# Kernel optimization log

Measured on AMD Instinct MI355X. Metric: run time of the kernel, lower is better.

The kernel has to match this reference:

```python
import jax, jax.numpy as jnp
import numpy as np

EPS = 1e-5
EMBED_DIM = 1024
CTX_DIM = 768
NUM_HEADS = 16
DH = EMBED_DIM // NUM_HEADS
# Faithful to torch source: embed_dim // num_heads ** 0.5 parses as embed_dim // (num_heads**0.5)
SCALE = EMBED_DIM // (NUM_HEADS ** 0.5)  # = 256.0


def ws_conv1x1(x, w, b, mask):
    # weight-standardized 1x1 conv1d: w [O, I, 1], x [B, I, T]
    w2 = w[..., 0]
    mu = jnp.mean(w2, axis=1, keepdims=True)
    var = jnp.var(w2, axis=1, keepdims=True)
    wn = (w2 - mu) * jax.lax.rsqrt(var + EPS)
    y = jnp.einsum('oi,bit->bot', wn, x) + b[None, :, None]
    if mask is not None:
        y = jnp.where(mask, y, 0.0)  # mask [B,1,T] bool
    return y


def layernorm(x, g, b):
    # normalize over last axis
    mu = jnp.mean(x, axis=-1, keepdims=True)
    var = jnp.var(x, axis=-1, keepdims=True)
    return (x - mu) * jax.lax.rsqrt(var + EPS) * g + b


def setup_inputs() -> dict:
    key = jax.random.key(0)
    ks = jax.random.split(key, 16)
    B, T, S = 4, 1024, 1024
    inp = {
        'x': jax.random.normal(ks[0], (B, EMBED_DIM, T), dtype=jnp.float32),
        'context': jax.random.normal(ks[1], (B, CTX_DIM, S), dtype=jnp.float32),
        'mask': jax.random.randint(ks[2], (B, 1, T), 0, 2).astype(bool),
        'mask_ctx': jax.random.randint(ks[3], (B, 1, S), 0, 2).astype(bool),
        'qw': jax.random.normal(ks[4], (EMBED_DIM, EMBED_DIM, 1), dtype=jnp.float32) * 0.02,
        'qb': jnp.zeros((EMBED_DIM,), jnp.float32),
        'kw': jax.random.normal(ks[5], (EMBED_DIM, CTX_DIM, 1), dtype=jnp.float32) * 0.02,
        'kb': jnp.zeros((EMBED_DIM,), jnp.float32),
        'vw': jax.random.normal(ks[6], (EMBED_DIM, CTX_DIM, 1), dtype=jnp.float32) * 0.02,
        'vb': jnp.zeros((EMBED_DIM,), jnp.float32),
        'ow': jax.random.normal(ks[7], (EMBED_DIM, EMBED_DIM, 1), dtype=jnp.float32) * 0.02,
        'ob': jnp.zeros((EMBED_DIM,), jnp.float32),
        'gq': jnp.ones((DH,), jnp.float32), 'bq': jnp.zeros((DH,), jnp.float32),
        'gk': jnp.ones((DH,), jnp.float32), 'bk': jnp.zeros((DH,), jnp.float32),
        'gv': jnp.ones((DH,), jnp.float32), 'bv': jnp.zeros((DH,), jnp.float32),
    }
    return inp


def reference(x, context, mask, mask_ctx, qw, qb, kw, kb, vw, vb, ow, ob, gq, bq, gk, bk, gv, bv):
    B, E, T = x.shape
    S = context.shape[-1]
    q = ws_conv1x1(x, qw, qb, mask)            # [B,E,T]
    k = ws_conv1x1(context, kw, kb, mask_ctx)  # [B,E,S]
    v = ws_conv1x1(context, vw, vb, mask_ctx)  # [B,E,S]
    # split heads -> [B,H,dh,L]
    q = q.reshape(B, NUM_HEADS, DH, T)
    k = k.reshape(B, NUM_HEADS, DH, S)
    v = v.reshape(B, NUM_HEADS, DH, S)
    # middle_norm: LayerNorm over dh (applied on transposed layout)
    q = jnp.swapaxes(layernorm(jnp.swapaxes(q, -1, -2), gq, bq), -1, -2)
    k = jnp.swapaxes(layernorm(jnp.swapaxes(k, -1, -2), gk, bk), -1, -2)
    v = jnp.swapaxes(layernorm(jnp.swapaxes(v, -1, -2), gv, bv), -1, -2)
    # scores: k^T @ q -> [B,H,S,T]
    scores = jnp.einsum('bhds,bhdt->bhst', k, q) / SCALE
    scores = jnp.where(mask[:, :, None, :], scores, -1e9)  # mask over query dim T
    scores = jax.nn.softmax(scores, axis=-1)               # softmax over T (as in source)
    scores = jnp.where(mask_ctx[:, :, :, None], scores, 0.0)
    out = jnp.einsum('bhds,bhst->bhdt', v, scores)          # v @ scores -> [B,H,dh,T]
    out = out.reshape(B, E, T)
    out = ws_conv1x1(out, ow, ob, mask) + x
    return out
```

## Files before the change

### kernel.cpp

```cpp
#include <hip/hip_runtime.h>

#define NB 4
#define TT 1024
#define SS 1024
#define EE 1024
#define CCH 768
#define NH 16
#define DHH 64
#define EPSF 1e-5f
#define QSCALE (1.4426950408889634f / 256.0f)

typedef unsigned short u16;
typedef __attribute__((ext_vector_type(8))) short short8;
typedef __attribute__((ext_vector_type(8))) unsigned short u16x8;
typedef __attribute__((ext_vector_type(4))) unsigned short u16x4;
typedef __attribute__((ext_vector_type(4))) float f32x4;

__device__ __forceinline__ u16 f2bu(float f) {
    union { float f; unsigned u; } x; x.f = f;
    unsigned r = x.u + 0x7fffu + ((x.u >> 16) & 1u);
    return (u16)(r >> 16);
}
__device__ __forceinline__ float bu2f(u16 u) {
    union { unsigned u; float f; } x; x.u = ((unsigned)u) << 16; return x.f;
}

#if __has_builtin(__builtin_amdgcn_exp2f)
#define EXP2(x) __builtin_amdgcn_exp2f(x)
#else
#define EXP2(x) exp2f(x)
#endif

#define MFMA16(a, b, c) __builtin_amdgcn_mfma_f32_16x16x32_bf16((a), (b), (c), 0, 0, 0)

#define PREP_WS_END   4096
#define PREP_SCAN_END (PREP_WS_END + 8)
#define PREP_TR_END   (PREP_SCAN_END + 1792)
#define PREP_FILL_END (PREP_TR_END + 4096)

__global__ __launch_bounds__(256) void prep(
    const float* __restrict__ qw, const float* __restrict__ kw,
    const float* __restrict__ vw, const float* __restrict__ ow,
    u16* __restrict__ wqn, u16* __restrict__ wkn,
    u16* __restrict__ wvn, u16* __restrict__ won,
    const float* __restrict__ x, const float* __restrict__ ctx,
    const int* __restrict__ mask, const int* __restrict__ mask_ctx,
    u16* __restrict__ xc, u16* __restrict__ cc,
    int* __restrict__ tIdx, int* __restrict__ sIdx,
    int* __restrict__ cntQ, int* __restrict__ cntK,
    float* __restrict__ outF) {
    __shared__ float tile[64][65];
    __shared__ int spos[64], smask[64], wtoti[4];
    __shared__ float sa[4], sb2[4], smean, srstd;
    int bid = blockIdx.x, tid = threadIdx.x;

    if (bid < PREP_WS_END) {
        int mat = bid >> 10, row = bid & 1023;
        const float* w = mat == 0 ? qw : (mat == 1 ? kw : (mat == 2 ? vw : ow));
        u16* wn = mat == 0 ? wqn : (mat == 1 ? wkn : (mat == 2 ? wvn : won));
        int I = (mat == 1 || mat == 2) ? CCH : EE;
        const float* wr = w + (size_t)row * I;
        float s = 0.f, s2 = 0.f;
        for (int i = tid; i < I; i += 256) { float v = wr[i]; s += v; s2 += v * v; }
#pragma unroll
        for (int off = 32; off > 0; off >>= 1) { s += __shfl_down(s, off); s2 += __shfl_down(s2, off); }
        int wid = tid >> 6;
        if ((tid & 63) == 0) { sa[wid] = s; sb2[wid] = s2; }
        __syncthreads();
        if (tid == 0) {
            float ts = sa[0] + sa[1] + sa[2] + sa[3];
            float ts2 = sb2[0] + sb2[1] + sb2[2] + sb2[3];
            float mean = ts / (float)I;
            float var = ts2 / (float)I - mean * mean;
            smean = mean; srstd = rsqrtf(var + EPSF);
        }
        __syncthreads();
        float mean = smean, r = srstd;
        u16* wo = wn + (size_t)row * I;
        for (int i = tid; i < I; i += 256) wo[i] = f2bu((wr[i] - mean) * r);
        return;
    }
    if (bid < PREP_SCAN_END) {
        int t = bid - PREP_WS_END;
        int which = t & 1, b = t >> 1;
        const int* m = (which ? mask_ctx : mask) + b * 1024;
        int* idx = (which ? sIdx : tIdx) + b * 1024;
        int* cnt = (which ? cntK : cntQ) + b;
        int base = tid * 4;
        int v[4]; int s = 0;
#pragma unroll
        for (int i = 0; i < 4; i++) { v[i] = m[base + i] ? 1 : 0; s += v[i]; }
        int lane = tid & 63, wid = tid >> 6;
        int inc = s;
#pragma unroll
        for (int off = 1; off < 64; off <<= 1) {
            int o = __shfl_up(inc, off);
            if (lane >= off) inc += o;
        }
        if (lane == 63) wtoti[wid] = inc;
        __syncthreads();
        int woff = 0;
        for (int i = 0; i < wid; i++) woff += wtoti[i];
        int p = woff + inc - s;
#pragma unroll
        for (int i = 0; i < 4; i++) {
            if (v[i]) idx[p] = base + i;
            p += v[i];
        }
        if (tid == 255) *cnt = p;
        return;
    }
    if (bid < PREP_TR_END) {
        int t = bid - PREP_SCAN_END;
        int xb = t & 15; int rem = t >> 4;
        int yy = rem % 28, b = rem / 28;
        int mat = yy < 16 ? 0 : 1;
        int r0 = (mat == 0 ? yy : yy - 16) * 64;
        int R = mat == 0 ? EE : CCH;
        const float* in = mat == 0 ? x : ctx;
        const int* m = (mat == 0 ? mask : mask_ctx) + (size_t)b * 1024;
        u16* out = mat == 0 ? xc : cc;
        int c0 = xb * 64;
        const float* ip = in + (size_t)b * R * 1024;
        u16* op = out + (size_t)b * R * 1024;
#pragma unroll
        for (int mm = 0; mm < 16; mm++) {
            int id = tid + 256 * mm; int r = id >> 6, c = id & 63;
            tile[r][c] = ip[(size_t)(r0 + r) * 1024 + c0 + c];
        }
        int base = tid * 4;
        int v[4]; int s = 0;
#pragma unroll
        for (int i = 0; i < 4; i++) { v[i] = m[base + i] ? 1 : 0; s += v[i]; }
        int lane = tid & 63, wid = tid >> 6;
        int inc = s;
#pragma unroll
        for (int off = 1; off < 64; off <<= 1) {
            int o = __shfl_up(inc, off);
            if (lane >= off) inc += o;
        }
        if (lane == 63) wtoti[wid] = inc;
        __syncthreads();
        int woff = 0;
        for (int i = 0; i < wid; i++) woff += wtoti[i];
        int p = woff + inc - s;
#pragma unroll
        for (int i = 0; i < 4; i++) {
            int g = base + i;
            if (g >= c0 && g < c0 + 64) { spos[g - c0] = p; smask[g - c0] = v[i]; }
            p += v[i];
        }
        __syncthreads();
#pragma unroll
        for (int mm = 0; mm < 16; mm++) {
            int id = tid + 256 * mm; int rr = id >> 6, cc2 = id & 63;
            if (smask[rr])
                op[(size_t)spos[rr] * R + r0 + cc2] = f2bu(tile[cc2][rr]);
        }
        return;
    }
    {
        int f = bid - PREP_TR_END;
        int b = f >> 10, o = f & 1023;
        const float* xr = x + ((size_t)b * EE + o) * TT;
        float* orow = outF + ((size_t)b * EE + o) * TT;
        const int* mrow = mask + (size_t)b * TT;
        int4 mv = ((const int4*)mrow)[tid];
        float4 xv = ((const float4*)xr)[tid];
        int t4 = tid * 4;
        if (!mv.x) orow[t4 + 0] = xv.x;
        if (!mv.y) orow[t4 + 1] = xv.y;
        if (!mv.z) orow[t4 + 2] = xv.z;
        if (!mv.w) orow[t4 + 3] = xv.w;
    }
}

__device__ __forceinline__ void gemm_core(
    const u16* __restrict__ A, const u16* __restrict__ Bp, int I,
    int o0, int l0, u16 (*at)[72], u16 (*bt)[72], f32x4 (&acc)[4][2]) {
    int tid = threadIdx.x;
    int w = tid >> 6, lane = tid & 63, quad = lane >> 4, l16 = lane & 15;
    int wm = w & 1, wn = w >> 1;
    int rA = tid >> 3, cA = (tid & 7) * 8;
    u16x8 ra[2][4], rb[2][2];
#pragma unroll
    for (int p = 0; p < 2; p++) {
        int kb = p * 64;
#pragma unroll
        for (int m = 0; m < 4; m++)
            ra[p][m] = *(const u16x8*)&A[(size_t)(o0 + rA + 32 * m) * I + kb + cA];
#pragma unroll
        for (int m = 0; m < 2; m++)
            rb[p][m] = *(const u16x8*)&Bp[(size_t)(l0 + rA + 32 * m) * I + kb + cA];
    }
    for (int k0 = 0; k0 < I; k0 += 128) {
#pragma unroll
        for (int half = 0; half < 2; half++) {
            __syncthreads();
#pragma unroll
            for (int m = 0; m < 4; m++) *(u16x8*)&at[rA + 32 * m][cA] = ra[half][m];
#pragma unroll
            for (int m = 0; m < 2; m++) *(u16x8*)&bt[rA + 32 * m][cA] = rb[half][m];
            __syncthreads();
            int kpre = k0 + half * 64 + 128;
            if (kpre < I) {
#pragma unroll
                for (int m = 0; m < 4; m++)
                    ra[half][m] = *(const u16x8*)&A[(size_t)(o0 + rA + 32 * m) * I + kpre + cA];
#pragma unroll
                for (int m = 0; m < 2; m++)
                    rb[half][m] = *(const u16x8*)&Bp[(size_t)(l0 + rA + 32 * m) * I + kpre + cA];
            }
#pragma unroll
            for (int ks = 0; ks < 64; ks += 32) {
                short8 af[4], bf[2];
#pragma unroll
                for (int i = 0; i < 4; i++)
                    af[i] = *(const short8*)&at[wm * 64 + i * 16 + l16][ks + quad * 8];
#pragma unroll
                for (int j = 0; j < 2; j++)
                    bf[j] = *(const short8*)&bt[wn * 32 + j * 16 + l16][ks + quad * 8];
#pragma unroll
                for (int mt = 0; mt < 4; mt++)
#pragma unroll
                    for (int nt = 0; nt < 2; nt++)
                        acc[mt][nt] = MFMA16(af[mt], bf[nt], acc[mt][nt]);
            }
        }
    }
}

__device__ __forceinline__ void gemm_core64(
    const u16* __restrict__ A, const u16* __restrict__ Bp, int I,
    int o0, int l0, u16 (*at)[72], u16 (*bt)[72], f32x4 (&acc)[4]) {
    int tid = threadIdx.x;
    int w = tid >> 6, lane = tid & 63, quad = lane >> 4, l16 = lane & 15;
    int rA = tid >> 3, cA = (tid & 7) * 8;
    u16x8 ra[2][2], rb[2][2];
#pragma unroll
    for (int p = 0; p < 2; p++) {
        int kb = p * 64;
#pragma unroll
        for (int m = 0; m < 2; m++) {
            ra[p][m] = *(const u16x8*)&A[(size_t)(o0 + rA + 32 * m) * I + kb + cA];
            rb[p][m] = *(const u16x8*)&Bp[(size_t)(l0 + rA + 32 * m) * I + kb + cA];
        }
    }
    for (int k0 = 0; k0 < I; k0 += 128) {
#pragma unroll
        for (int half = 0; half < 2; half++) {
            __syncthreads();
#pragma unroll
            for (int m = 0; m < 2; m++) {
                *(u16x8*)&at[rA + 32 * m][cA] = ra[half][m];
                *(u16x8*)&bt[rA + 32 * m][cA] = rb[half][m];
            }
            __syncthreads();
            int kpre = k0 + half * 64 + 128;
            if (kpre < I) {
#pragma unroll
                for (int m = 0; m < 2; m++) {
                    ra[half][m] = *(const u16x8*)&A[(size_t)(o0 + rA + 32 * m) * I + kpre + cA];
                    rb[half][m] = *(const u16x8*)&Bp[(size_t)(l0 + rA + 32 * m) * I + kpre + cA];
                }
            }
#pragma unroll
            for (int ks = 0; ks < 64; ks += 32) {
                short8 bf = *(const short8*)&bt[w * 16 + l16][ks + quad * 8];
#pragma unroll
                for (int mt = 0; mt < 4; mt++) {
                    short8 af = *(const short8*)&at[mt * 16 + l16][ks + quad * 8];
                    acc[mt] = MFMA16(af, bf, acc[mt]);
                }
            }
        }
    }
}

__global__ __launch_bounds__(256) void proj_qkv(
    const u16* __restrict__ wq, const u16* __restrict__ wk, const u16* __restrict__ wv,
    const u16* __restrict__ xc, const u16* __restrict__ cc,
    const float* __restrict__ qb, const float* __restrict__ kb, const float* __restrict__ vbi,
    const int* __restrict__ cntQ, const int* __restrict__ cntK,
    const float* __restrict__ gq, const float* __restrict__ bq,
    const float* __restrict__ gk, const float* __restrict__ bk,
    u16* __restrict__ qc, u16* __restrict__ kc, u16* __restrict__ yv) {
    int mat = blockIdx.x >> 3;
    int o0 = (blockIdx.x & 7) * 128;
    int l0 = blockIdx.y * 64;
    int b = blockIdx.z;
    int limit = (mat == 0) ? cntQ[b] : cntK[b];
    if (l0 >= limit) return;
    __shared__ u16 at[128][72];
    __shared__ u16 bt[64][72];
    __shared__ float sg[64], sbe[64], sbias[128];
    int tid = threadIdx.x;
    int w = tid >> 6, lane = tid & 63, quad = lane >> 4, l16 = lane & 15;
    int wm = w & 1, wn = w >> 1;
    const u16* A = mat == 0 ? wq : (mat == 1 ? wk : wv);
    const u16* BT = mat == 0 ? xc : cc;
    const float* bias = mat == 0 ? qb : (mat == 1 ? kb : vbi);
    int I = mat == 0 ? EE : CCH;
    if (mat < 2 && tid < 64) {
        sg[tid] = (mat == 0 ? gq : gk)[tid];
        sbe[tid] = (mat == 0 ? bq : bk)[tid];
    }
    if (tid < 128) sbias[tid] = bias[o0 + tid];

    f32x4 acc[4][2] = {};
    gemm_core(A, BT + (size_t)b * 1024 * I, I, o0, l0, at, bt, acc);

    if (mat < 2) {
        u16* outT = mat == 0 ? qc : kc;
        float scale = mat == 0 ? QSCALE : 1.0f;
        int h = (o0 >> 6) + wm;
        int bh = b * NH + h;
#pragma unroll
        for (int nt = 0; nt < 2; nt++) {
            int l = l0 + wn * 32 + nt * 16 + l16;
            float vbuf[16];
            float s = 0.f;
#pragma unroll
            for (int mt = 0; mt < 4; mt++)
#pragma unroll
                for (int reg = 0; reg < 4; reg++) {
                    float v = acc[mt][nt][reg] + sbias[wm * 64 + mt * 16 + quad * 4 + reg];
                    vbuf[mt * 4 + reg] = v; s += v;
                }
            s += __shfl_xor(s, 16); s += __shfl_xor(s, 32);
            float mean = s * (1.f / 64);
            float s2 = 0.f;
#pragma unroll
            for (int i = 0; i < 16; i++) { float dv = vbuf[i] - mean; s2 += dv * dv; }
            s2 += __shfl_xor(s2, 16); s2 += __shfl_xor(s2, 32);
            float r = rsqrtf(s2 * (1.f / 64) + EPSF);
            if (l < limit) {
                u16* op = outT + ((size_t)bh * 1024 + l) * 64;
#pragma unroll
                for (int mt = 0; mt < 4; mt++) {
                    u16x4 pk;
#pragma unroll
                    for (int reg = 0; reg < 4; reg++) {
                        int d = mt * 16 + quad * 4 + reg;
                        pk[reg] = f2bu(((vbuf[mt * 4 + reg] - mean) * r * sg[d] + sbe[d]) * scale);
                    }
                    *(u16x4*)&op[mt * 16 + quad * 4] = pk;
                }
            }
        }
    } else {
#pragma unroll
        for (int nt = 0; nt < 2; nt++) {
            int l = l0 + wn * 32 + nt * 16 + l16;
            if (l < limit) {
#pragma unroll
                for (int mt = 0; mt < 4; mt++)
#pragma unroll
                    for (int reg = 0; reg < 4; reg++) {
                        int o = o0 + wm * 64 + mt * 16 + quad * 4 + reg;
                        float v = acc[mt][nt][reg] + sbias[wm * 64 + mt * 16 + quad * 4 + reg];
                        yv[((size_t)b * EE + o) * 1024 + l] = f2bu(v);
                    }
            }
        }
    }
}

__global__ __launch_bounds__(256) void attn_stats_mfma(
    const u16* __restrict__ qc, const u16* __restrict__ kc,
    const int* __restrict__ cntQ, const int* __restrict__ cntK,
    const float* __restrict__ gv, const float* __restrict__ bv,
    const u16* __restrict__ yv, u16* __restrict__ vc) {
    int s0 = blockIdx.x * 64, h = blockIdx.y, b = blockIdx.z;
    int Sc = cntK[b], Tc = cntQ[b];
    if (s0 >= Sc) return;
    __shared__ u16 kt[64][72];
    __shared__ u16 qt[64][72];
    __shared__ float lp[4][64];
    int tid = threadIdx.x;
    int w = tid >> 6, lane = tid & 63, quad = lane >> 4, l16 = lane & 15;
    int head = b * NH + h;
    const u16* kp = kc + (size_t)head * SS * DHH;
    const u16* qp = qc + (size_t)head * TT * DHH;
    int rA = tid >> 3, cA = (tid & 7) * 8;
#pragma unroll
    for (int m = 0; m < 2; m++)
        *(u16x8*)&kt[rA + 32 * m][cA] = *(const u16x8*)&kp[(size_t)(s0 + rA + 32 * m) * DHH + cA];
    u16x8 rq[2][2];
#pragma unroll
    for (int p = 0; p < 2; p++)
#pragma unroll
        for (int m = 0; m < 2; m++)
            rq[p][m] = *(const u16x8*)&qp[(size_t)(p * 64 + rA + 32 * m) * DHH + cA];
    float rl[4][4] = {};
    for (int t0 = 0; t0 < Tc; t0 += 128) {
#pragma unroll
        for (int half = 0; half < 2; half++) {
            int tb = t0 + half * 64;
            __syncthreads();
#pragma unroll
            for (int m = 0; m < 2; m++) *(u16x8*)&qt[rA + 32 * m][cA] = rq[half][m];
            __syncthreads();
            int tpre = tb + 128;
            if (tpre < TT) {
#pragma unroll
                for (int m = 0; m < 2; m++)
                    rq[half][m] = *(const u16x8*)&qp[(size_t)(tpre + rA + 32 * m) * DHH + cA];
            }
            int tcol = tb + w * 16 + l16;
            f32x4 acc[4] = {};
#pragma unroll
            for (int ks = 0; ks < 64; ks += 32) {
                short8 bf = *(const short8*)&qt[w * 16 + l16][ks + quad * 8];
#pragma unroll
                for (int mt = 0; mt < 4; mt++) {
                    short8 af = *(const short8*)&kt[mt * 16 + l16][ks + quad * 8];
                    acc[mt] = MFMA16(af, bf, acc[mt]);
                }
            }
            if (tcol < Tc) {
#pragma unroll
                for (int mt = 0; mt < 4; mt++)
#pragma unroll
                    for (int reg = 0; reg < 4; reg++)
                        rl[mt][reg] += EXP2(acc[mt][reg]);
            }
        }
    }
#pragma unroll
    for (int mt = 0; mt < 4; mt++) {
#pragma unroll
        for (int reg = 0; reg < 4; reg++) {
            float v = rl[mt][reg];
            v += __shfl_xor(v, 1); v += __shfl_xor(v, 2);
            v += __shfl_xor(v, 4); v += __shfl_xor(v, 8);
            if (l16 == 0) lp[w][mt * 16 + quad * 4 + reg] = v;
        }
    }
    __syncthreads();
    if (tid < 64 && s0 + tid < Sc) {
        int spos = s0 + tid;
        float lv = lp[0][tid] + lp[1][tid] + lp[2][tid] + lp[3][tid];
        float wsc = lv > 0.f ? (1.f / lv) : 0.f;
        const u16* vin = yv + ((size_t)b * EE + h * 64) * SS + spos;
        u16* vout = vc + ((size_t)b * EE + h * 64) * SS + spos;
        float sm = 0.f, s2 = 0.f;
        float vals[DHH];
#pragma unroll
        for (int d = 0; d < DHH; d++) {
            float v = bu2f(vin[(size_t)d * SS]);
            vals[d] = v; sm += v; s2 += v * v;
        }
        float mean = sm * (1.f / DHH);
        float var = s2 * (1.f / DHH) - mean * mean;
        float r = rsqrtf(var + EPSF);
#pragma unroll
        for (int d = 0; d < DHH; d++)
            vout[(size_t)d * SS] = f2bu(((vals[d] - mean) * r * gv[d] + bv[d]) * wsc);
    }
}

__global__ __launch_bounds__(256) void attn_pv_mfma(
    const u16* __restrict__ qc, const u16* __restrict__ kc, const u16* __restrict__ vc,
    const int* __restrict__ cntQ, const int* __restrict__ cntK,
    u16* __restrict__ ac) {
    int t0 = blockIdx.x * 64, h = blockIdx.y, b = blockIdx.z;
    int Tc = cntQ[b], Sc = cntK[b];
    if (t0 >= Tc) return;
    __shared__ u16 qt[64][72];
    __shared__ u16 kt[64][72];
    __shared__ u16 vt[64][72];
    __shared__ u16 pt[64][72];
    int tid = threadIdx.x;
    int w = tid >> 6, lane = tid & 63, quad = lane >> 4, l16 = lane & 15;
    int head = b * NH + h;
    const u16* qp = qc + (size_t)head * TT * DHH;
    const u16* kp = kc + (size_t)head * SS * DHH;
    const u16* vp = vc + ((size_t)head * DHH) * SS;
    int rA = tid >> 3, cA = (tid & 7) * 8;
#pragma unroll
    for (int m = 0; m < 2; m++)
        *(u16x8*)&qt[rA + 32 * m][cA] = *(const u16x8*)&qp[(size_t)(t0 + rA + 32 * m) * DHH + cA];
    u16x8 rk[2][2], rv[2][2];
#pragma unroll
    for (int p = 0; p < 2; p++)
#pragma unroll
        for (int m = 0; m < 2; m++) {
            rk[p][m] = *(const u16x8*)&kp[(size_t)(p * 64 + rA + 32 * m) * DHH + cA];
            rv[p][m] = *(const u16x8*)&vp[(size_t)(rA + 32 * m) * SS + p * 64 + cA];
        }
    int tl = w * 16 + l16;

    f32x4 oacc[4] = {};
    for (int s0 = 0; s0 < Sc; s0 += 128) {
#pragma unroll
        for (int half = 0; half < 2; half++) {
            int sb = s0 + half * 64;
            if (sb >= Sc) break;
            __syncthreads();
#pragma unroll
            for (int m = 0; m < 2; m++) {
                *(u16x8*)&kt[rA + 32 * m][cA] = rk[half][m];
                *(u16x8*)&vt[rA + 32 * m][cA] = rv[half][m];
            }
            __syncthreads();
            int spre = sb + 128;
            if (spre < SS) {
#pragma unroll
                for (int m = 0; m < 2; m++) {
                    rk[half][m] = *(const u16x8*)&kp[(size_t)(spre + rA + 32 * m) * DHH + cA];
                    rv[half][m] = *(const u16x8*)&vp[(size_t)(rA + 32 * m) * SS + spre + cA];
                }
            }
            f32x4 acc[4] = {};
#pragma unroll
            for (int ks = 0; ks < 64; ks += 32) {
                short8 bf = *(const short8*)&qt[tl][ks + quad * 8];
#pragma unroll
                for (int mt = 0; mt < 4; mt++) {
                    short8 af = *(const short8*)&kt[mt * 16 + l16][ks + quad * 8];
                    acc[mt] = MFMA16(af, bf, acc[mt]);
                }
            }
#pragma unroll
            for (int mt = 0; mt < 4; mt++) {
                u16x4 pk;
#pragma unroll
                for (int reg = 0; reg < 4; reg++) {
                    int sl = mt * 16 + quad * 4 + reg;
                    pk[reg] = (sb + sl < Sc) ? f2bu(EXP2(acc[mt][reg])) : (u16)0;
                }
                *(u16x4*)&pt[tl][mt * 16 + quad * 4] = pk;
            }
#pragma unroll
            for (int ks = 0; ks < 64; ks += 32) {
                short8 bf = *(const short8*)&pt[tl][ks + quad * 8];
#pragma unroll
                for (int mt = 0; mt < 4; mt++) {
                    short8 af = *(const short8*)&vt[mt * 16 + l16][ks + quad * 8];
                    oacc[mt] = MFMA16(af, bf, oacc[mt]);
                }
            }
        }
    }
    __syncthreads();
#pragma unroll
    for (int mt = 0; mt < 4; mt++) {
        u16x4 pk;
#pragma unroll
        for (int reg = 0; reg < 4; reg++) pk[reg] = f2bu(oacc[mt][reg]);
        *(u16x4*)&pt[tl][mt * 16 + quad * 4] = pk;
    }
    __syncthreads();
#pragma unroll
    for (int i = 0; i < 2; i++) {
        int id = tid * 2 + i;
        int r = id >> 3, c = (id & 7) * 8;
        if (t0 + r < Tc)
            *(u16x8*)&ac[((size_t)b * TT + t0 + r) * EE + h * 64 + c] =
                *(const u16x8*)&pt[r][c];
    }
}

__global__ __launch_bounds__(256) void proj_o(
    const u16* __restrict__ won, const u16* __restrict__ ac,
    const float* __restrict__ obi, const int* __restrict__ tIdx,
    const int* __restrict__ cntQ, const float* __restrict__ x,
    float* __restrict__ out) {
    int o0 = blockIdx.x * 64, l0 = blockIdx.y * 64, b = blockIdx.z;
    int Tc = cntQ[b];
    if (l0 >= Tc) return;
    __shared__ u16 at[64][72];
    __shared__ u16 bt[64][72];
    __shared__ float sbias[64];
    __shared__ int stre[64];
    int tid = threadIdx.x;
    int w = tid >> 6, lane = tid & 63, quad = lane >> 4, l16 = lane & 15;
    if (tid < 64) {
        sbias[tid] = obi[o0 + tid];
        stre[tid] = tIdx[(size_t)b * 1024 + l0 + tid];
    }
    f32x4 acc[4] = {};
    gemm_core64(won, ac + (size_t)b * TT * EE, EE, o0, l0, at, bt, acc);
    int l = l0 + w * 16 + l16;
    if (l < Tc) {
        int treal = stre[w * 16 + l16];
#pragma unroll
        for (int mt = 0; mt < 4; mt++)
#pragma unroll
            for (int reg = 0; reg < 4; reg++) {
                int o = o0 + mt * 16 + quad * 4 + reg;
                size_t off = ((size_t)b * EE + o) * TT + treal;
                out[off] = acc[mt][reg] + sbias[mt * 16 + quad * 4 + reg] + x[off];
            }
    }
}

extern "C" void kernel_launch(void* const* d_in, const int* in_sizes, int n_in,
                              void* d_out, int out_size, void* d_ws, size_t ws_size,
                              hipStream_t stream) {
    const float* x        = (const float*)d_in[0];
    const float* ctx      = (const float*)d_in[1];
    const int*   mask     = (const int*)d_in[2];
    const int*   mask_ctx = (const int*)d_in[3];
    const float* qw  = (const float*)d_in[4];
    const float* qbi = (const float*)d_in[5];
    const float* kw  = (const float*)d_in[6];
    const float* kbi = (const float*)d_in[7];
    const float* vw  = (const float*)d_in[8];
    const float* vbi = (const float*)d_in[9];
    const float* ow  = (const float*)d_in[10];
    const float* obi = (const float*)d_in[11];
    const float* gq = (const float*)d_in[12];
    const float* bq = (const float*)d_in[13];
    const float* gk = (const float*)d_in[14];
    const float* bk = (const float*)d_in[15];
    const float* gv = (const float*)d_in[16];
    const float* bv = (const float*)d_in[17];

    u16* p = (u16*)d_ws;
    u16* wqn = p; p += (size_t)EE * EE;
    u16* wkn = p; p += (size_t)EE * CCH;
    u16* wvn = p; p += (size_t)EE * CCH;
    u16* won = p; p += (size_t)EE * EE;
    u16* xc  = p; p += (size_t)NB * TT * EE;
    u16* cc  = p; p += (size_t)NB * SS * CCH;
    u16* yv  = p; p += (size_t)NB * EE * SS;
    u16* qc  = p; p += (size_t)NB * NH * TT * DHH;
    u16* kc  = p; p += (size_t)NB * NH * SS * DHH;
    u16* vc  = p; p += (size_t)NB * EE * SS;
    u16* ac  = p; p += (size_t)NB * TT * EE;
    int* tIdx = (int*)p;
    int* sIdx = tIdx + NB * 1024;
    int* cntQ = sIdx + NB * 1024;
    int* cntK = cntQ + NB;

    prep<<<PREP_FILL_END, 256, 0, stream>>>(
        qw, kw, vw, ow, wqn, wkn, wvn, won, x, ctx, mask, mask_ctx,
        xc, cc, tIdx, sIdx, cntQ, cntK, (float*)d_out);

    proj_qkv<<<dim3(24, 16, NB), 256, 0, stream>>>(
        wqn, wkn, wvn, xc, cc, qbi, kbi, vbi, cntQ, cntK,
        gq, bq, gk, bk, qc, kc, yv);

    attn_stats_mfma<<<dim3(16, NH, NB), 256, 0, stream>>>(
        qc, kc, cntQ, cntK, gv, bv, yv, vc);

    attn_pv_mfma<<<dim3(16, NH, NB), 256, 0, stream>>>(
        qc, kc, vc, cntQ, cntK, ac);

    proj_o<<<dim3(16, 16, NB), 256, 0, stream>>>(
        won, ac, obi, tIdx, cntQ, x, (float*)d_out);
}
```

Before: 223.1 us.

## Fuse V layernorm into projection, fold softmax denominator into exp, widen proj_o tile

The V layernorm moves into the proj_qkv epilogue, alongside Q and K, so the stats kernel no longer reads yv and writes a separately normalized vc copy. The stats kernel now writes only the per-row negative log2 of the softmax denominator, which attn_pv adds inside the exp2 instead of pre-scaling V. proj_o switches to the 128x64 gemm_core tile with half as many blocks. Together these remove one full V read/write pass and some kernel work, at the cost of more shared memory in attn_pv and fewer blocks in proj_o. The lneg indexing relies on a 'head' variable being defined in attn_stats.

```diff
diff --git a/kernel.cpp b/kernel.cpp
--- a/kernel.cpp
+++ b/kernel.cpp
@@ -230,53 +230,6 @@
     }
 }
 
-__device__ __forceinline__ void gemm_core64(
-    const u16* __restrict__ A, const u16* __restrict__ Bp, int I,
-    int o0, int l0, u16 (*at)[72], u16 (*bt)[72], f32x4 (&acc)[4]) {
-    int tid = threadIdx.x;
-    int w = tid >> 6, lane = tid & 63, quad = lane >> 4, l16 = lane & 15;
-    int rA = tid >> 3, cA = (tid & 7) * 8;
-    u16x8 ra[2][2], rb[2][2];
-#pragma unroll
-    for (int p = 0; p < 2; p++) {
-        int kb = p * 64;
-#pragma unroll
-        for (int m = 0; m < 2; m++) {
-            ra[p][m] = *(const u16x8*)&A[(size_t)(o0 + rA + 32 * m) * I + kb + cA];
-            rb[p][m] = *(const u16x8*)&Bp[(size_t)(l0 + rA + 32 * m) * I + kb + cA];
-        }
-    }
-    for (int k0 = 0; k0 < I; k0 += 128) {
-#pragma unroll
-        for (int half = 0; half < 2; half++) {
-            __syncthreads();
-#pragma unroll
-            for (int m = 0; m < 2; m++) {
-                *(u16x8*)&at[rA + 32 * m][cA] = ra[half][m];
-                *(u16x8*)&bt[rA + 32 * m][cA] = rb[half][m];
-            }
-            __syncthreads();
-            int kpre = k0 + half * 64 + 128;
-            if (kpre < I) {
-#pragma unroll
-                for (int m = 0; m < 2; m++) {
-                    ra[half][m] = *(const u16x8*)&A[(size_t)(o0 + rA + 32 * m) * I + kpre + cA];
-                    rb[half][m] = *(const u16x8*)&Bp[(size_t)(l0 + rA + 32 * m) * I + kpre + cA];
-                }
-            }
-#pragma unroll
-            for (int ks = 0; ks < 64; ks += 32) {
-                short8 bf = *(const short8*)&bt[w * 16 + l16][ks + quad * 8];
-#pragma unroll
-                for (int mt = 0; mt < 4; mt++) {
-                    short8 af = *(const short8*)&at[mt * 16 + l16][ks + quad * 8];
-                    acc[mt] = MFMA16(af, bf, acc[mt]);
-                }
-            }
-        }
-    }
-}
-
 __global__ __launch_bounds__(256) void proj_qkv(
     const u16* __restrict__ wq, const u16* __restrict__ wk, const u16* __restrict__ wv,
     const u16* __restrict__ xc, const u16* __restrict__ cc,
@@ -284,7 +237,8 @@
     const int* __restrict__ cntQ, const int* __restrict__ cntK,
     const float* __restrict__ gq, const float* __restrict__ bq,
     const float* __restrict__ gk, const float* __restrict__ bk,
-    u16* __restrict__ qc, u16* __restrict__ kc, u16* __restrict__ yv) {
+    const float* __restrict__ gv, const float* __restrict__ bv,
+    u16* __restrict__ qc, u16* __restrict__ kc, u16* __restrict__ vn) {
     int mat = blockIdx.x >> 3;
     int o0 = (blockIdx.x & 7) * 128;
     int l0 = blockIdx.y * 64;
@@ -301,40 +255,42 @@
     const u16* BT = mat == 0 ? xc : cc;
     const float* bias = mat == 0 ? qb : (mat == 1 ? kb : vbi);
     int I = mat == 0 ? EE : CCH;
-    if (mat < 2 && tid < 64) {
-        sg[tid] = (mat == 0 ? gq : gk)[tid];
-        sbe[tid] = (mat == 0 ? bq : bk)[tid];
+    if (tid < 64) {
+        const float* gsrc = mat == 0 ? gq : (mat == 1 ? gk : gv);
+        const float* bsrc = mat == 0 ? bq : (mat == 1 ? bk : bv);
+        sg[tid] = gsrc[tid];
+        sbe[tid] = bsrc[tid];
     }
     if (tid < 128) sbias[tid] = bias[o0 + tid];
 
     f32x4 acc[4][2] = {};
     gemm_core(A, BT + (size_t)b * 1024 * I, I, o0, l0, at, bt, acc);
 
-    if (mat < 2) {
-        u16* outT = mat == 0 ? qc : kc;
-        float scale = mat == 0 ? QSCALE : 1.0f;
-        int h = (o0 >> 6) + wm;
-        int bh = b * NH + h;
-#pragma unroll
-        for (int nt = 0; nt < 2; nt++) {
-            int l = l0 + wn * 32 + nt * 16 + l16;
-            float vbuf[16];
-            float s = 0.f;
-#pragma unroll
-            for (int mt = 0; mt < 4; mt++)
-#pragma unroll
-                for (int reg = 0; reg < 4; reg++) {
-                    float v = acc[mt][nt][reg] + sbias[wm * 64 + mt * 16 + quad * 4 + reg];
-                    vbuf[mt * 4 + reg] = v; s += v;
-                }
-            s += __shfl_xor(s, 16); s += __shfl_xor(s, 32);
-            float mean = s * (1.f / 64);
-            float s2 = 0.f;
-#pragma unroll
-            for (int i = 0; i < 16; i++) { float dv = vbuf[i] - mean; s2 += dv * dv; }
-            s2 += __shfl_xor(s2, 16); s2 += __shfl_xor(s2, 32);
-            float r = rsqrtf(s2 * (1.f / 64) + EPSF);
-            if (l < limit) {
+    float scale = mat == 0 ? QSCALE : 1.0f;
+    int h = (o0 >> 6) + wm;
+    int bh = b * NH + h;
+#pragma unroll
+    for (int nt = 0; nt < 2; nt++) {
+        int l = l0 + wn * 32 + nt * 16 + l16;
+        float vbuf[16];
+        float s = 0.f;
+#pragma unroll
+        for (int mt = 0; mt < 4; mt++)
+#pragma unroll
+            for (int reg = 0; reg < 4; reg++) {
+                float v = acc[mt][nt][reg] + sbias[wm * 64 + mt * 16 + quad * 4 + reg];
+                vbuf[mt * 4 + reg] = v; s += v;
+            }
+        s += __shfl_xor(s, 16); s += __shfl_xor(s, 32);
+        float mean = s * (1.f / 64);
+        float s2 = 0.f;
+#pragma unroll
+        for (int i = 0; i < 16; i++) { float dv = vbuf[i] - mean; s2 += dv * dv; }
+        s2 += __shfl_xor(s2, 16); s2 += __shfl_xor(s2, 32);
+        float r = rsqrtf(s2 * (1.f / 64) + EPSF);
+        if (l < limit) {
+            if (mat < 2) {
+                u16* outT = mat == 0 ? qc : kc;
                 u16* op = outT + ((size_t)bh * 1024 + l) * 64;
 #pragma unroll
                 for (int mt = 0; mt < 4; mt++) {
@@ -346,20 +302,14 @@
                     }
                     *(u16x4*)&op[mt * 16 + quad * 4] = pk;
                 }
-            }
-        }
-    } else {
-#pragma unroll
-        for (int nt = 0; nt < 2; nt++) {
-            int l = l0 + wn * 32 + nt * 16 + l16;
-            if (l < limit) {
+            } else {
 #pragma unroll
                 for (int mt = 0; mt < 4; mt++)
 #pragma unroll
                     for (int reg = 0; reg < 4; reg++) {
-                        int o = o0 + wm * 64 + mt * 16 + quad * 4 + reg;
-                        float v = acc[mt][nt][reg] + sbias[wm * 64 + mt * 16 + quad * 4 + reg];
-                        yv[((size_t)b * EE + o) * 1024 + l] = f2bu(v);
+                        int d = mt * 16 + quad * 4 + reg;
+                        vn[((size_t)b * EE + h * 64 + d) * 1024 + l] =
+                            f2bu((vbuf[mt * 4 + reg] - mean) * r * sg[d] + sbe[d]);
                     }
             }
         }
@@ -369,8 +319,7 @@
 __global__ __launch_bounds__(256) void attn_stats_mfma(
     const u16* __restrict__ qc, const u16* __restrict__ kc,
     const int* __restrict__ cntQ, const int* __restrict__ cntK,
-    const float* __restrict__ gv, const float* __restrict__ bv,
-    const u16* __restrict__ yv, u16* __restrict__ vc) {
+    float* __restrict__ lneg) {
     int s0 = blockIdx.x * 64, h = blockIdx.y, b = blockIdx.z;
     int Sc = cntK[b], Tc = cntQ[b];
     if (s0 >= Sc) return;
@@ -439,31 +388,15 @@
     }
     __syncthreads();
     if (tid < 64 && s0 + tid < Sc) {
-        int spos = s0 + tid;
         float lv = lp[0][tid] + lp[1][tid] + lp[2][tid] + lp[3][tid];
-        float wsc = lv > 0.f ? (1.f / lv) : 0.f;
-        const u16* vin = yv + ((size_t)b * EE + h * 64) * SS + spos;
-        u16* vout = vc + ((size_t)b * EE + h * 64) * SS + spos;
-        float sm = 0.f, s2 = 0.f;
-        float vals[DHH];
-#pragma unroll
-        for (int d = 0; d < DHH; d++) {
-            float v = bu2f(vin[(size_t)d * SS]);
-            vals[d] = v; sm += v; s2 += v * v;
-        }
-        float mean = sm * (1.f / DHH);
-        float var = s2 * (1.f / DHH) - mean * mean;
-        float r = rsqrtf(var + EPSF);
-#pragma unroll
-        for (int d = 0; d < DHH; d++)
-            vout[(size_t)d * SS] = f2bu(((vals[d] - mean) * r * gv[d] + bv[d]) * wsc);
+        lneg[(size_t)head * SS + s0 + tid] = -log2f(fmaxf(lv, 1e-30f));
     }
 }
 
 __global__ __launch_bounds__(256) void attn_pv_mfma(
-    const u16* __restrict__ qc, const u16* __restrict__ kc, const u16* __restrict__ vc,
+    const u16* __restrict__ qc, const u16* __restrict__ kc, const u16* __restrict__ vn,
     const int* __restrict__ cntQ, const int* __restrict__ cntK,
-    u16* __restrict__ ac) {
+    const float* __restrict__ lneg, u16* __restrict__ ac) {
     int t0 = blockIdx.x * 64, h = blockIdx.y, b = blockIdx.z;
     int Tc = cntQ[b], Sc = cntK[b];
     if (t0 >= Tc) return;
@@ -471,13 +404,15 @@
     __shared__ u16 kt[64][72];
     __shared__ u16 vt[64][72];
     __shared__ u16 pt[64][72];
+    __shared__ float sln[SS];
     int tid = threadIdx.x;
     int w = tid >> 6, lane = tid & 63, quad = lane >> 4, l16 = lane & 15;
     int head = b * NH + h;
     const u16* qp = qc + (size_t)head * TT * DHH;
     const u16* kp = kc + (size_t)head * SS * DHH;
-    const u16* vp = vc + ((size_t)head * DHH) * SS;
+    const u16* vp = vn + ((size_t)head * DHH) * SS;
     int rA = tid >> 3, cA = (tid & 7) * 8;
+    for (int i = tid; i < SS; i += 256) sln[i] = lneg[(size_t)head * SS + i];
 #pragma unroll
     for (int m = 0; m < 2; m++)
         *(u16x8*)&qt[rA + 32 * m][cA] = *(const u16x8*)&qp[(size_t)(t0 + rA + 32 * m) * DHH + cA];
@@ -528,7 +463,7 @@
 #pragma unroll
                 for (int reg = 0; reg < 4; reg++) {
                     int sl = mt * 16 + quad * 4 + reg;
-                    pk[reg] = (sb + sl < Sc) ? f2bu(EXP2(acc[mt][reg])) : (u16)0;
+                    pk[reg] = (sb + sl < Sc) ? f2bu(EXP2(acc[mt][reg] + sln[sb + sl])) : (u16)0;
                 }
                 *(u16x4*)&pt[tl][mt * 16 + quad * 4] = pk;
             }
@@ -567,32 +502,35 @@
     const float* __restrict__ obi, const int* __restrict__ tIdx,
     const int* __restrict__ cntQ, const float* __restrict__ x,
     float* __restrict__ out) {
-    int o0 = blockIdx.x * 64, l0 = blockIdx.y * 64, b = blockIdx.z;
+    int o0 = blockIdx.x * 128, l0 = blockIdx.y * 64, b = blockIdx.z;
     int Tc = cntQ[b];
     if (l0 >= Tc) return;
-    __shared__ u16 at[64][72];
+    __shared__ u16 at[128][72];
     __shared__ u16 bt[64][72];
-    __shared__ float sbias[64];
+    __shared__ float sbias[128];
     __shared__ int stre[64];
     int tid = threadIdx.x;
     int w = tid >> 6, lane = tid & 63, quad = lane >> 4, l16 = lane & 15;
-    if (tid < 64) {
-        sbias[tid] = obi[o0 + tid];
-        stre[tid] = tIdx[(size_t)b * 1024 + l0 + tid];
-    }
-    f32x4 acc[4] = {};
-    gemm_core64(won, ac + (size_t)b * TT * EE, EE, o0, l0, at, bt, acc);
-    int l = l0 + w * 16 + l16;
-    if (l < Tc) {
-        int treal = stre[w * 16 + l16];
-#pragma unroll
-        for (int mt = 0; mt < 4; mt++)
-#pragma unroll
-            for (int reg = 0; reg < 4; reg++) {
-                int o = o0 + mt * 16 + quad * 4 + reg;
-                size_t off = ((size_t)b * EE + o) * TT + treal;
-                out[off] = acc[mt][reg] + sbias[mt * 16 + quad * 4 + reg] + x[off];
-            }
+    int wm = w & 1, wn = w >> 1;
+    if (tid < 128) sbias[tid] = obi[o0 + tid];
+    if (tid < 64) stre[tid] = tIdx[(size_t)b * 1024 + l0 + tid];
+    f32x4 acc[4][2] = {};
+    gemm_core(won, ac + (size_t)b * TT * EE, EE, o0, l0, at, bt, acc);
+#pragma unroll
+    for (int nt = 0; nt < 2; nt++) {
+        int lcol = wn * 32 + nt * 16 + l16;
+        int l = l0 + lcol;
+        if (l < Tc) {
+            int treal = stre[lcol];
+#pragma unroll
+            for (int mt = 0; mt < 4; mt++)
+#pragma unroll
+                for (int reg = 0; reg < 4; reg++) {
+                    int o = o0 + wm * 64 + mt * 16 + quad * 4 + reg;
+                    size_t off = ((size_t)b * EE + o) * TT + treal;
+                    out[off] = acc[mt][nt][reg] + sbias[wm * 64 + mt * 16 + quad * 4 + reg] + x[off];
+                }
+        }
     }
 }
 
@@ -625,11 +563,11 @@
     u16* won = p; p += (size_t)EE * EE;
     u16* xc  = p; p += (size_t)NB * TT * EE;
     u16* cc  = p; p += (size_t)NB * SS * CCH;
-    u16* yv  = p; p += (size_t)NB * EE * SS;
+    u16* vn  = p; p += (size_t)NB * EE * SS;
     u16* qc  = p; p += (size_t)NB * NH * TT * DHH;
     u16* kc  = p; p += (size_t)NB * NH * SS * DHH;
-    u16* vc  = p; p += (size_t)NB * EE * SS;
     u16* ac  = p; p += (size_t)NB * TT * EE;
+    float* lneg = (float*)p; p += (size_t)NB * NH * SS * 2;
     int* tIdx = (int*)p;
     int* sIdx = tIdx + NB * 1024;
     int* cntQ = sIdx + NB * 1024;
@@ -641,14 +579,14 @@
 
     proj_qkv<<<dim3(24, 16, NB), 256, 0, stream>>>(
         wqn, wkn, wvn, xc, cc, qbi, kbi, vbi, cntQ, cntK,
-        gq, bq, gk, bk, qc, kc, yv);
+        gq, bq, gk, bk, gv, bv, qc, kc, vn);
 
     attn_stats_mfma<<<dim3(16, NH, NB), 256, 0, stream>>>(
-        qc, kc, cntQ, cntK, gv, bv, yv, vc);
+        qc, kc, cntQ, cntK, lneg);
 
     attn_pv_mfma<<<dim3(16, NH, NB), 256, 0, stream>>>(
-        qc, kc, vc, cntQ, cntK, ac);
-
-    proj_o<<<dim3(16, 16, NB), 256, 0, stream>>>(
+        qc, kc, vn, cntQ, cntK, lneg, ac);
+
+    proj_o<<<dim3(8, 16, NB), 256, 0, stream>>>(
         won, ac, obi, tIdx, cntQ, x, (float*)d_out);
 }
```

New measurement: 226.0 us. Within noise of the previous version (+1.3%).
